# Optimization experiments

Measured on AMD Instinct MI355X. Metric: run time of the kernel, lower is better.

## Reference

```python
import jax, jax.numpy as jnp
import numpy as np

N, E, F, H, C, G = 100000, 800000, 128, 128, 10, 128
EPS = 1e-5


def setup_inputs() -> dict:
    key = jax.random.key(0)
    ks = jax.random.split(key, 8)
    return {
        "x": jax.random.normal(ks[0], (N, F), jnp.float32),
        "edge_index": jax.random.randint(ks[1], (2, E), 0, N),
        "batch": jnp.sort(jax.random.randint(ks[2], (N,), 0, G)),
        "edge_weight": jax.random.uniform(ks[3], (E,), jnp.float32, 0.1, 1.0),
        "bn_feat_w": jnp.ones((F,), jnp.float32),
        "bn_feat_b": jnp.full((F,), 1e-4, jnp.float32),
        "conv_feat_W": jax.random.normal(ks[4], (F, H), jnp.float32) / np.float32(np.sqrt(F)),
        "conv_feat_b": jnp.zeros((H,), jnp.float32),
        "bns_w": jnp.ones((3, H), jnp.float32),
        "bns_b": jnp.full((3, H), 1e-4, jnp.float32),
        "convs_W": jax.random.normal(ks[5], (3, H, H), jnp.float32) / np.float32(np.sqrt(H)),
        "convs_b": jnp.zeros((3, H), jnp.float32),
        "bn_fc_w": jnp.ones((H,), jnp.float32),
        "bn_fc_b": jnp.full((H,), 1e-4, jnp.float32),
        "lin_fc_W": jax.random.normal(ks[6], (H, H), jnp.float32) / np.float32(np.sqrt(H)),
        "lin_fc_b": jnp.zeros((H,), jnp.float32),
        "bn_hidden_w": jnp.ones((H,), jnp.float32),
        "bn_hidden_b": jnp.full((H,), 1e-4, jnp.float32),
        "lin_class_W": jax.random.normal(ks[7], (H, C), jnp.float32) / np.float32(np.sqrt(H)),
        "lin_class_b": jnp.zeros((C,), jnp.float32),
    }


def _bn(h, w, b):
    # training-mode BatchNorm1d: biased batch stats over dim 0
    mu = h.mean(0)
    var = jnp.mean((h - mu) ** 2, 0)
    return (h - mu) * jax.lax.rsqrt(var + EPS) * w + b


def reference(x, edge_index, batch, edge_weight,
              bn_feat_w, bn_feat_b, conv_feat_W, conv_feat_b,
              bns_w, bns_b, convs_W, convs_b,
              bn_fc_w, bn_fc_b, lin_fc_W, lin_fc_b,
              bn_hidden_w, bn_hidden_b, lin_class_W, lin_class_b):
    n = x.shape[0]
    loops = jnp.arange(n)
    # PyG GCNConv: add self-loops (weight 1) + symmetric normalization, shared by all convs
    row = jnp.concatenate([edge_index[0], loops])
    col = jnp.concatenate([edge_index[1], loops])
    ew = jnp.concatenate([edge_weight, jnp.ones((n,), x.dtype)])
    deg = jax.ops.segment_sum(ew, col, num_segments=n)
    dinv = jnp.where(deg > 0, jax.lax.rsqrt(jnp.maximum(deg, EPS)), 0.0)
    norm = (dinv[row] * ew * dinv[col])[:, None]  # [E+N, 1]

    def conv(h, W, b):
        m = (h @ W)[row] * norm                 # gather + scale per edge
        return jax.ops.segment_sum(m, col, num_segments=n) + b

    h = _bn(x, bn_feat_w, bn_feat_b)
    h = jax.nn.relu(conv(h, conv_feat_W, conv_feat_b))
    h_init = h

    x_list = []
    # branch 1: BN -> Conv -> ReLU chain
    h = h_init
    for i in range(3):
        h = jax.nn.relu(conv(_bn(h, bns_w[i], bns_b[i]), convs_W[i], convs_b[i]))
    x_list.append(h)
    # branch 2: double application of the same BN/Conv per step
    h = h_init
    for i in range(3):
        h_ = jax.nn.relu(conv(_bn(h, bns_w[i], bns_b[i]), convs_W[i], convs_b[i]))
        h = jax.nn.relu(conv(_bn(h_, bns_w[i], bns_b[i]), convs_W[i], convs_b[i]))
    x_list.append(h)
    # branch 3: identical to branch 1 when conv_residual=False
    h = h_init
    for i in range(3):
        h = jax.nn.relu(conv(_bn(h, bns_w[i], bns_b[i]), convs_W[i], convs_b[i]))
    x_list.append(h)
    # branch 4: BN -> ReLU only
    h = h_init
    for i in range(3):
        h = jax.nn.relu(_bn(h, bns_w[i], bns_b[i]))
    x_list.append(h)

    def head(hn):
        g = jax.ops.segment_sum(hn, batch, num_segments=G)  # global_add_pool
        g = jax.nn.relu(_bn(g, bn_fc_w, bn_fc_b) @ lin_fc_W + lin_fc_b)
        g = _bn(g, bn_hidden_w, bn_hidden_b)
        return jax.nn.log_softmax(g @ lin_class_W + lin_class_b, axis=-1)

    return tuple(head(hn) for hn in x_list)
```

## Files before the change

### kernel.cpp

```cpp
#include <hip/hip_runtime.h>

#define N_NODES 100000
#define NPAD    100032
#define NBLK    1563
#define NEDGE   800000
#define NGRP    128
#define NSLOT   32
#define EPS     1e-5f

typedef unsigned int   u32;
typedef unsigned short u16;
typedef short bf16x8 __attribute__((ext_vector_type(8)));
typedef float f32x4  __attribute__((ext_vector_type(4)));

__device__ __forceinline__ float bf2f(u32 u){ return __uint_as_float(u << 16); }
__device__ __forceinline__ u16 f2bf(float f){
  u32 x = __float_as_uint(f);
  x += 0x7fffu + ((x >> 16) & 1u);
  return (u16)(x >> 16);
}

__global__ void k_init(float* deg, int* cnt, int* fill, float* gbuf){
  int i = blockIdx.x * 256 + threadIdx.x;
  if (i < NPAD){ deg[i] = 1.0f; cnt[i] = 0; fill[i] = 0; }
  if (i < 4 * NGRP * 128) gbuf[i] = 0.f;
}

__global__ void k_deg(const int* __restrict__ col, const float* __restrict__ ew,
                      float* __restrict__ deg, int* __restrict__ cnt){
  int e = blockIdx.x * 256 + threadIdx.x;
  if (e < NEDGE){
    int c = col[e];
    atomicAdd(&deg[c], ew[e]);
    atomicAdd(&cnt[c], 1);
  }
}

__global__ void k_dinv(const float* __restrict__ deg, float* __restrict__ dinv, float* __restrict__ srow){
  int i = blockIdx.x * 256 + threadIdx.x;
  if (i < N_NODES){
    float d = deg[i];
    float v = d > 0.f ? rsqrtf(fmaxf(d, EPS)) : 0.f;
    dinv[i] = v; srow[i] = v * v;
  }
}

__global__ __launch_bounds__(256) void k_chunksum(const int* __restrict__ cnt, int* __restrict__ csum){
  int b = blockIdx.x, t = threadIdx.x;
  int s = 0;
  for (int i = t; i < 1024; i += 256){ int idx = b * 1024 + i; if (idx < N_NODES) s += cnt[idx]; }
  __shared__ int red[256];
  red[t] = s; __syncthreads();
  for (int o = 128; o > 0; o >>= 1){ if (t < o) red[t] += red[t + o]; __syncthreads(); }
  if (t == 0) csum[b] = red[0];
}

__global__ __launch_bounds__(128) void k_chunkscan(const int* __restrict__ csum, int* __restrict__ coff,
                                                   int* __restrict__ ptrA){
  int t = threadIdx.x;
  __shared__ int s[128];
  int v = (t < 98) ? csum[t] : 0;
  s[t] = v; __syncthreads();
  for (int o = 1; o < 128; o <<= 1){
    int x = (t >= o) ? s[t - o] : 0;
    __syncthreads(); s[t] += x; __syncthreads();
  }
  if (t < 98) coff[t] = s[t] - v;
  if (t == 0) ptrA[N_NODES] = NEDGE;
}

__global__ __launch_bounds__(256) void k_scan2(const int* __restrict__ cnt, const int* __restrict__ coff,
                                               int* __restrict__ ptrA){
  int b = blockIdx.x, t = threadIdx.x;
  int base = b * 1024 + t * 4;
  int v[4], tot = 0;
  #pragma unroll
  for (int k = 0; k < 4; k++){ int idx = base + k; v[k] = (idx < N_NODES) ? cnt[idx] : 0; tot += v[k]; }
  __shared__ int sc[256];
  sc[t] = tot; __syncthreads();
  for (int o = 1; o < 256; o <<= 1){
    int x = (t >= o) ? sc[t - o] : 0;
    __syncthreads(); sc[t] += x; __syncthreads();
  }
  int off = coff[b] + sc[t] - tot;
  #pragma unroll
  for (int k = 0; k < 4; k++){ int idx = base + k; if (idx < N_NODES) ptrA[idx] = off; off += v[k]; }
}

__global__ void k_fill(const int* __restrict__ row, const int* __restrict__ col,
                       const float* __restrict__ ew, const float* __restrict__ dinv,
                       const int* __restrict__ ptrA, int* __restrict__ fill, int2* __restrict__ adj,
                       float* __restrict__ srow){
  int e = blockIdx.x * 256 + threadIdx.x;
  if (e < NEDGE){
    int r = row[e], c = col[e];
    float w = dinv[r] * ew[e] * dinv[c];
    int pos = ptrA[c] + atomicAdd(&fill[c], 1);
    adj[pos] = make_int2(r, __float_as_int(w));
    atomicAdd(&srow[c], w);
  }
}

__global__ __launch_bounds__(256) void k_bhist(const int* __restrict__ batch, int* __restrict__ bpart){
  __shared__ int loc[128];
  int t = threadIdx.x;
  if (t < 128) loc[t] = 0;
  __syncthreads();
  int i = blockIdx.x * 256 + t;
  if (i < N_NODES) atomicAdd(&loc[batch[i]], 1);
  __syncthreads();
  if (t < 128) bpart[blockIdx.x * 128 + t] = loc[t];
}

__global__ __launch_bounds__(128) void k_bscan(const int* __restrict__ bpart, int* __restrict__ gptr){
  int t = threadIdx.x;
  int v = 0;
  for (int p = 0; p < 391; p++) v += bpart[p * 128 + t];
  __shared__ int s[128];
  s[t] = v; __syncthreads();
  for (int o = 1; o < 128; o <<= 1){
    int x = (t >= o) ? s[t - o] : 0;
    __syncthreads(); s[t] += x; __syncthreads();
  }
  gptr[t + 1] = s[t];
  if (t == 0) gptr[0] = 0;
}

__global__ __launch_bounds__(256) void k_cvtstats(const float* __restrict__ x, u32* __restrict__ dst,
                                                  float* __restrict__ sums_out){
  __shared__ float R[1024];
  int t = threadIdx.x;
  float s0 = 0.f, q0 = 0.f, s1 = 0.f, q1 = 0.f;
  size_t base = (size_t)blockIdx.x * 4096 + t;
  #pragma unroll
  for (int it = 0; it < 16; it++){
    size_t idx = base + (size_t)it * 256;
    if (idx < (size_t)N_NODES * 64){
      float2 v = ((const float2*)x)[idx];
      dst[idx] = (u32)f2bf(v.x) | ((u32)f2bf(v.y) << 16);
      s0 += v.x; q0 += v.x * v.x; s1 += v.y; q1 += v.y * v.y;
    }
  }
  R[t] = s0; R[256 + t] = q0; R[512 + t] = s1; R[768 + t] = q1;
  __syncthreads();
  if (t < 64){
    float S0 = 0.f, Q0 = 0.f, S1 = 0.f, Q1 = 0.f;
    #pragma unroll
    for (int g = 0; g < 4; g++){
      S0 += R[g * 64 + t];       Q0 += R[256 + g * 64 + t];
      S1 += R[512 + g * 64 + t]; Q1 += R[768 + g * 64 + t];
    }
    float* so = sums_out + (blockIdx.x & (NSLOT - 1)) * 256;
    atomicAdd(&so[2 * t], S0);
    atomicAdd(&so[2 * t + 1], S1);
    atomicAdd(&so[128 + 2 * t], Q0);
    atomicAdd(&so[128 + 2 * t + 1], Q1);
  }
}

__device__ __forceinline__ void fold_body(int blk, int t, const float* __restrict__ sums,
    const float* __restrict__ bw, const float* __restrict__ bb,
    const float* __restrict__ W, const float* __restrict__ bias,
    u16* __restrict__ Wh, u16* __restrict__ Wl, float* __restrict__ rb,
    float* scl, float* shf, float* stot, float* rred){
  {
    float s = 0.f;
    #pragma unroll 4
    for (int sl = 0; sl < NSLOT; sl++) s += sums[sl * 256 + t];
    stot[t] = s;
  }
  __syncthreads();
  if (t < 128){
    float mu  = stot[t] * (1.f / N_NODES);
    float var = stot[128 + t] * (1.f / N_NODES) - mu * mu;
    float sc  = bw[t] * rsqrtf(var + EPS);
    scl[t] = sc; shf[t] = bb[t] - mu * sc;
  }
  __syncthreads();
  {
    int idx = blk * 256 + t;
    int lane_ = idx & 63, sl = idx >> 6;
    int nt_ = sl >> 2, ks_ = sl & 3;
    int n_ = nt_ * 16 + (lane_ & 15);
    int kb = ks_ * 32 + (lane_ >> 4) * 8;
    u16 hi8[8], lo8[8];
    #pragma unroll
    for (int j = 0; j < 8; j++){
      float wv = W[(kb + j) * 128 + n_];
      float xv = scl[kb + j] * wv;
      u16 hh = f2bf(xv);
      hi8[j] = hh; lo8[j] = f2bf(xv - bf2f(hh));
    }
    uint4 ph, pl;
    ph.x = (u32)hi8[0] | ((u32)hi8[1] << 16); ph.y = (u32)hi8[2] | ((u32)hi8[3] << 16);
    ph.z = (u32)hi8[4] | ((u32)hi8[5] << 16); ph.w = (u32)hi8[6] | ((u32)hi8[7] << 16);
    pl.x = (u32)lo8[0] | ((u32)lo8[1] << 16); pl.y = (u32)lo8[2] | ((u32)lo8[3] << 16);
    pl.z = (u32)lo8[4] | ((u32)lo8[5] << 16); pl.w = (u32)lo8[6] | ((u32)lo8[7] << 16);
    *(uint4*)&Wh[idx * 8] = ph;
    *(uint4*)&Wl[idx * 8] = pl;
  }
  {
    int nl = t & 15, kk = t >> 4;
    int n2 = blk * 16 + nl;
    float rp = 0.f;
    #pragma unroll
    for (int j = 0; j < 8; j++){
      int k2 = kk * 8 + j;
      rp += shf[k2] * W[k2 * 128 + n2];
    }
    rred[t] = rp;
  }
  __syncthreads();
  if (t < 16){
    float s = 0.f;
    #pragma unroll
    for (int kk2 = 0; kk2 < 16; kk2++) s += rred[kk2 * 16 + t];
    int n2 = blk * 16 + t;
    rb[n2] = s;
    rb[128 + n2] = bias[n2];
  }
}

__global__ __launch_bounds__(256) void k_fold(const float* __restrict__ sums,
    const float* __restrict__ bw, const float* __restrict__ bb,
    const float* __restrict__ W, const float* __restrict__ bias,
    u16* __restrict__ Wh, u16* __restrict__ Wl, float* __restrict__ rb){
  __shared__ float scl[128], shf[128], stot[256], rred[256];
  fold_body(blockIdx.x, threadIdx.x, sums, bw, bb, W, bias, Wh, Wl, rb, scl, shf, stot, rred);
}

__global__ __launch_bounds__(256) void k_fold2(
    const float* __restrict__ sumsA, const float* __restrict__ bwA, const float* __restrict__ bbA,
    const float* __restrict__ WA, const float* __restrict__ biasA,
    u16* __restrict__ WhA, u16* __restrict__ WlA, float* __restrict__ rbA,
    const float* __restrict__ sumsB, const float* __restrict__ bwB, const float* __restrict__ bbB,
    const float* __restrict__ WB, const float* __restrict__ biasB,
    u16* __restrict__ WhB, u16* __restrict__ WlB, float* __restrict__ rbB){
  __shared__ float scl[128], shf[128], stot[256], rred[256];
  int bb_ = blockIdx.x;
  if (bb_ < 8)
    fold_body(bb_, threadIdx.x, sumsA, bwA, bbA, WA, biasA, WhA, WlA, rbA, scl, shf, stot, rred);
  else
    fold_body(bb_ - 8, threadIdx.x, sumsB, bwB, bbB, WB, biasB, WhB, WlB, rbB, scl, shf, stot, rred);
}

#define CONV_EPILOGUE(RB, HOUT, SOUT, BLK)                                     \
  __syncthreads();                                                             \
  sred[t] = 0.f;                                                               \
  __syncthreads();                                                             \
  _Pragma("unroll")                                                            \
  for (int nt = 0; nt < 8; nt++){                                              \
    int colc = nt * 16 + m;                                                    \
    float rv = RB[colc], bv = RB[128 + colc];                                  \
    float s = 0.f, qq = 0.f;                                                   \
    _Pragma("unroll")                                                          \
    for (int r = 0; r < 4; r++){                                               \
      int rown = row0 + q * 4 + r;                                             \
      float v = C[nt][r] + srow[rown] * rv + bv;                               \
      v = fmaxf(v, 0.f);                                                       \
      u16 sv = f2bf(v);                                                        \
      HOUT[(size_t)rown * 128 + colc] = sv;                                    \
      if (rown < N_NODES){ float vv = bf2f(sv); s += vv; qq += vv * vv; }      \
    }                                                                          \
    s  += __shfl_xor(s, 16, 64);  s  += __shfl_xor(s, 32, 64);                 \
    qq += __shfl_xor(qq, 16, 64); qq += __shfl_xor(qq, 32, 64);                \
    if (q == 0){                                                               \
      atomicAdd(&sred[colc], s);                                               \
      atomicAdd(&sred[128 + colc], qq);                                        \
    }                                                                          \
  }                                                                            \
  __syncthreads();                                                             \
  atomicAdd(&SOUT[((BLK) & (NSLOT - 1)) * 256 + t], sred[t]);

#define FMA_KS(KS, V, WT) \
  acc[KS][0] += (WT) * __uint_as_float((V).x << 16); acc[KS][1] += (WT) * __uint_as_float((V).x & 0xffff0000u); \
  acc[KS][2] += (WT) * __uint_as_float((V).y << 16); acc[KS][3] += (WT) * __uint_as_float((V).y & 0xffff0000u); \
  acc[KS][4] += (WT) * __uint_as_float((V).z << 16); acc[KS][5] += (WT) * __uint_as_float((V).z & 0xffff0000u); \
  acc[KS][6] += (WT) * __uint_as_float((V).w << 16); acc[KS][7] += (WT) * __uint_as_float((V).w & 0xffff0000u);

#define VMCNT6() asm volatile("s_waitcnt vmcnt(6)" ::: "memory")
#define VMCNT5() asm volatile("s_waitcnt vmcnt(5)" ::: "memory")
#define SB0()    __builtin_amdgcn_sched_barrier(0)


__device__ __forceinline__ void gll_stage(const u16* __restrict__ h, u16* dst, int2 aj, int lane){
  int c = lane & 15, g = lane >> 4;
  #pragma unroll
  for (int ii = 0; ii < 4; ii++){
    int rl = ii * 4 + g;
    int srcrow = __shfl(aj.x, rl, 64);
    const u16* src = h + (size_t)srcrow * 128 + (size_t)((c ^ rl) * 8);
    __builtin_amdgcn_global_load_lds((const void*)src, (void*)(dst + ii * 512), 16, 0, 0);
  }
}

#define GITER(WA, WB, WC, WD, STG, J)                                          \
  WD = *(const int2*)(adj + base_ + min((J) + 3, dcl));                        \
  VMCNT6();                                                                    \
  {                                                                            \
    float wgt = __int_as_float(__shfl((WA).y, m, 64));                         \
    if ((J) < deg){                                                            \
      const u16* sp = stage + (STG) * 2048;                                    \
      _Pragma("unroll")                                                        \
      for (int ks = 0; ks < 4; ks++){                                          \
        int slot = (q + 4 * ks) ^ m;                                           \
        uint4 v = *(const uint4*)(sp + m * 128 + slot * 8);                    \
        FMA_KS(ks, v, wgt)                                                     \
      }                                                                        \
    }                                                                          \
  }                                                                            \
  VMCNT5();                                                                    \
  gll_stage(h, stage + (STG) * 2048, WC, lane);                                \
  SB0();

__device__ __forceinline__ void gather_row_lds(const u16* __restrict__ h,
    const int* __restrict__ ptrA, const int2* __restrict__ adj,
    const float* __restrict__ dinv, int row0, int lane, u16* stage,
    float (&acc)[4][8]){
  int m = lane & 15, q = lane >> 4;
  #pragma unroll
  for (int ks = 0; ks < 4; ks++)
    #pragma unroll
    for (int j = 0; j < 8; j++) acc[ks][j] = 0.f;
  int r = row0 + m;
  int r2 = min(r, N_NODES - 1);
  int b0 = ptrA[r2], b1 = ptrA[r2 + 1];
  int deg = (r < N_NODES) ? (b1 - b0) : 0;
  int base_ = b0;
  int dcl = max(deg - 1, 0);
  float di = dinv[r2];
  float sw = (r < N_NODES) ? di * di : 0.f;
  const u16* hq = h + q * 8;
  const u16* sp_ = hq + (size_t)r2 * 128;
  uint4 s0 = *(const uint4*)(sp_);
  uint4 s1 = *(const uint4*)(sp_ + 32);
  uint4 s2 = *(const uint4*)(sp_ + 64);
  uint4 s3 = *(const uint4*)(sp_ + 96);
  int2 W0 = *(const int2*)(adj + base_);
  int2 W1 = *(const int2*)(adj + base_ + min(1, dcl));
  int wmax = deg;
  wmax = max(wmax, __shfl_xor(wmax, 1, 64));
  wmax = max(wmax, __shfl_xor(wmax, 2, 64));
  wmax = max(wmax, __shfl_xor(wmax, 4, 64));
  wmax = max(wmax, __shfl_xor(wmax, 8, 64));
  FMA_KS(0, s0, sw) FMA_KS(1, s1, sw) FMA_KS(2, s2, sw) FMA_KS(3, s3, sw)
  if (wmax > 0){
    int2 W2 = W0, W3 = W0;
    SB0();
    gll_stage(h, stage, W0, lane);
    SB0();
    W2 = *(const int2*)(adj + base_ + min(2, dcl));
    SB0();
    gll_stage(h, stage + 2048, W1, lane);
    SB0();
    for (int j0 = 0; j0 < wmax; j0 += 4){
      GITER(W0, W1, W2, W3, 0, j0)
      GITER(W1, W2, W3, W0, 1, j0 + 1)
      GITER(W2, W3, W0, W1, 0, j0 + 2)
      GITER(W3, W0, W1, W2, 1, j0 + 3)
    }
  }
}

#define BUILD_AFRAG()                                                          \
  bf16x8 AH[4], AL[4];                                                         \
  _Pragma("unroll")                                                            \
  for (int ks = 0; ks < 4; ks++)                                               \
    _Pragma("unroll")                                                          \
    for (int j = 0; j < 8; j++){                                               \
      u16 hh = f2bf(acc[ks][j]);                                               \
      AH[ks][j] = (short)hh;                                                   \
      AL[ks][j] = (short)f2bf(acc[ks][j] - bf2f(hh));                          \
    }

#define MFMA_3PASS(WH, WL_)                                                    \
  _Pragma("unroll")                                                            \
  for (int ks = 0; ks < 4; ks++){                                              \
    _Pragma("unroll")                                                          \
    for (int nt = 0; nt < 8; nt++){                                            \
      bf16x8 bh = ((const bf16x8*)WH)[(nt * 4 + ks) * 64 + lane];              \
      bf16x8 bl = ((const bf16x8*)WL_)[(nt * 4 + ks) * 64 + lane];             \
      C[nt] = __builtin_amdgcn_mfma_f32_16x16x32_bf16(AH[ks], bh, C[nt], 0, 0, 0); \
      C[nt] = __builtin_amdgcn_mfma_f32_16x16x32_bf16(AL[ks], bh, C[nt], 0, 0, 0); \
      C[nt] = __builtin_amdgcn_mfma_f32_16x16x32_bf16(AH[ks], bl, C[nt], 0, 0, 0); \
    }                                                                          \
  }

__global__ __launch_bounds__(256, 3) void k_conv(
    const u16* __restrict__ h, const int* __restrict__ ptrA, const int2* __restrict__ adj,
    const float* __restrict__ dinv, const float* __restrict__ srow,
    const u16* __restrict__ Wh, const u16* __restrict__ Wl, const float* __restrict__ rb,
    u16* __restrict__ hout, float* __restrict__ sums_out){
  __shared__ u16 hstage[4][2][2048];
  __shared__ float sred[256];
  int t = threadIdx.x;
  int wave = t >> 6, lane = t & 63, m = lane & 15, q = lane >> 4;
  int blk = blockIdx.x;
  int row0 = blk * 64 + wave * 16;
  float acc[4][8];
  gather_row_lds(h, ptrA, adj, dinv, row0, lane, &hstage[wave][0][0], acc);
  BUILD_AFRAG()
  f32x4 C[8];
  #pragma unroll
  for (int nt = 0; nt < 8; nt++) C[nt] = f32x4{0.f, 0.f, 0.f, 0.f};
  MFMA_3PASS(Wh, Wl)
  CONV_EPILOGUE(rb, hout, sums_out, blk)
}

__global__ __launch_bounds__(256, 3) void k_conv2(
    const u16* __restrict__ hA, const u16* __restrict__ hB,
    const int* __restrict__ ptrA, const int2* __restrict__ adj,
    const float* __restrict__ dinv, const float* __restrict__ srow,
    const u16* __restrict__ WhA, const u16* __restrict__ WlA, const float* __restrict__ rbA,
    u16* __restrict__ houtA, float* __restrict__ sumsA,
    const u16* __restrict__ WhB, const u16* __restrict__ WlB, const float* __restrict__ rbB,
    u16* __restrict__ houtB, float* __restrict__ sumsB){
  __shared__ u16 hstage[4][2][2048];
  __shared__ float sred[256];
  int t = threadIdx.x;
  int wave = t >> 6, lane = t & 63, m = lane & 15, q = lane >> 4;
  int bb = blockIdx.x;
  int second = bb >= NBLK;
  int blk = second ? bb - NBLK : bb;
  const u16* h = second ? hB : hA;
  const u16* Wh = second ? WhB : WhA;
  const u16* Wl = second ? WlB : WlA;
  const float* rb = second ? rbB : rbA;
  u16* hout = second ? houtB : houtA;
  float* sums_out = second ? sumsB : sumsA;
  int row0 = blk * 64 + wave * 16;
  float acc[4][8];
  gather_row_lds(h, ptrA, adj, dinv, row0, lane, &hstage[wave][0][0], acc);
  BUILD_AFRAG()
  f32x4 C[8];
  #pragma unroll
  for (int nt = 0; nt < 8; nt++) C[nt] = f32x4{0.f, 0.f, 0.f, 0.f};
  MFMA_3PASS(Wh, Wl)
  CONV_EPILOGUE(rb, hout, sums_out, blk)
}

__global__ __launch_bounds__(256, 3) void k_dualconv(
    const u16* __restrict__ h, const int* __restrict__ ptrA, const int2* __restrict__ adj,
    const float* __restrict__ dinv, const float* __restrict__ srow,
    const u16* __restrict__ Wh1, const u16* __restrict__ Wl1, const float* __restrict__ rb1,
    u16* __restrict__ hout1, float* __restrict__ sums1,
    const u16* __restrict__ Wh2, const u16* __restrict__ Wl2, const float* __restrict__ rb2,
    u16* __restrict__ hout2, float* __restrict__ sums2){
  __shared__ u16 hstage[4][2][2048];
  __shared__ float sred[256];
  int t = threadIdx.x;
  int wave = t >> 6, lane = t & 63, m = lane & 15, q = lane >> 4;
  int blk = blockIdx.x;
  int row0 = blk * 64 + wave * 16;
  float acc[4][8];
  gather_row_lds(h, ptrA, adj, dinv, row0, lane, &hstage[wave][0][0], acc);
  BUILD_AFRAG()
  f32x4 C[8];
  #pragma unroll
  for (int nt = 0; nt < 8; nt++) C[nt] = f32x4{0.f, 0.f, 0.f, 0.f};
  MFMA_3PASS(Wh1, Wl1)
  CONV_EPILOGUE(rb1, hout1, sums1, blk)
  #pragma unroll
  for (int nt = 0; nt < 8; nt++) C[nt] = f32x4{0.f, 0.f, 0.f, 0.f};
  MFMA_3PASS(Wh2, Wl2)
  CONV_EPILOGUE(rb2, hout2, sums2, blk)
}

__global__ __launch_bounds__(256) void k_normrelu(const u16* __restrict__ h, const float* __restrict__ sums,
    const float* __restrict__ bw, const float* __restrict__ bb, u16* __restrict__ o,
    float* __restrict__ sums_out){
  __shared__ float scl[128], shf[128], R[1024], stot[256];
  int t = threadIdx.x;
  {
    float s = 0.f;
    #pragma unroll 4
    for (int sl = 0; sl < NSLOT; sl++) s += sums[sl * 256 + t];
    stot[t] = s;
  }
  __syncthreads();
  if (t < 128){
    float mu  = stot[t] * (1.f / N_NODES);
    float var = stot[128 + t] * (1.f / N_NODES) - mu * mu;
    float sc  = bw[t] * rsqrtf(var + EPS);
    scl[t] = sc; shf[t] = bb[t] - mu * sc;
  }
  __syncthreads();
  int c0 = (t & 63) * 2;
  float sc0 = scl[c0], sh0 = shf[c0], sc1 = scl[c0 + 1], sh1 = shf[c0 + 1];
  float s0 = 0.f, q0 = 0.f, s1 = 0.f, q1 = 0.f;
  size_t base = (size_t)blockIdx.x * 4096 + t;
  #pragma unroll
  for (int it = 0; it < 16; it++){
    size_t idx = base + (size_t)it * 256;
    if (idx < (size_t)N_NODES * 64){
      u32 v = ((const u32*)h)[idx];
      float x0 = fmaxf(bf2f(v & 0xffffu) * sc0 + sh0, 0.f);
      float x1 = fmaxf(bf2f(v >> 16) * sc1 + sh1, 0.f);
      u16 r0 = f2bf(x0), r1 = f2bf(x1);
      ((u32*)o)[idx] = (u32)r0 | ((u32)r1 << 16);
      float y0 = bf2f(r0), y1 = bf2f(r1);
      s0 += y0; q0 += y0 * y0; s1 += y1; q1 += y1 * y1;
    }
  }
  R[t] = s0; R[256 + t] = q0; R[512 + t] = s1; R[768 + t] = q1;
  __syncthreads();
  if (t < 64){
    float S0 = 0.f, Q0 = 0.f, S1 = 0.f, Q1 = 0.f;
    #pragma unroll
    for (int g = 0; g < 4; g++){
      S0 += R[g * 64 + t];       Q0 += R[256 + g * 64 + t];
      S1 += R[512 + g * 64 + t]; Q1 += R[768 + g * 64 + t];
    }
    float* so = sums_out + (blockIdx.x & (NSLOT - 1)) * 256;
    atomicAdd(&so[2 * t], S0);
    atomicAdd(&so[2 * t + 1], S1);
    atomicAdd(&so[128 + 2 * t], Q0);
    atomicAdd(&so[128 + 2 * t + 1], Q1);
  }
}

__global__ __launch_bounds__(128) void k_pool(const u16* __restrict__ h, const int* __restrict__ gptr,
                                              float* __restrict__ gdst){
  int g = blockIdx.x >> 3, s = blockIdx.x & 7, t = threadIdx.x;
  int b = gptr[g], e = gptr[g + 1];
  int len = e - b, per = (len + 7) >> 3;
  int r0 = b + s * per, r1 = min(r0 + per, e);
  float acc = 0.f;
  for (int r = r0; r < r1; r++) acc += bf2f(h[(size_t)r * 128 + t]);
  atomicAdd(&gdst[g * 128 + t], acc);
}

__global__ __launch_bounds__(256) void k_head(const float* __restrict__ gbuf,
    const float* __restrict__ fcw, const float* __restrict__ fcb,
    const float* __restrict__ Wfc, const float* __restrict__ bfc,
    const float* __restrict__ bhw, const float* __restrict__ bhb,
    const float* __restrict__ Wcl, const float* __restrict__ bcl,
    float* __restrict__ out){
  __shared__ float GS[128 * 65];
  __shared__ float ls[256], lq[256];
  __shared__ float scl[128], shf[128], scl2[128], shf2[128];
  __shared__ float sumT[128], sumQ[128];
  __shared__ float WclT[1280], Lrow[1280];
  int t = threadIdx.x, br = blockIdx.x;
  int slot = (br == 1) ? 1 : (br == 3 ? 3 : 0);
  const float* G = gbuf + slot * 16384;
  {
    int col = t & 127, hf2 = t >> 7;
    float s = 0.f, q = 0.f;
    for (int g = hf2 * 64; g < hf2 * 64 + 64; g++){ float v = G[g * 128 + col]; s += v; q += v * v; }
    ls[t] = s; lq[t] = q;
  }
  for (int idx = t; idx < 1280; idx += 256){
    int cc = idx >> 7, c = idx & 127;
    WclT[idx] = Wcl[c * 10 + cc];
  }
  if (t < 128){ sumT[t] = 0.f; sumQ[t] = 0.f; }
  __syncthreads();
  if (t < 128){
    float s = ls[t] + ls[t + 128], q = lq[t] + lq[t + 128];
    float mu = s * (1.f / 128), var = q * (1.f / 128) - mu * mu;
    float sc = fcw[t] * rsqrtf(var + EPS);
    scl[t] = sc; shf[t] = fcb[t] - mu * sc;
  }
  __syncthreads();
  int tr = t >> 4, tc = t & 15, r0 = tr * 8, c0 = tc * 8;
  float acc[8][8];
  #pragma unroll
  for (int a = 0; a < 8; a++)
    #pragma unroll
    for (int b = 0; b < 8; b++) acc[a][b] = 0.f;
  for (int kh = 0; kh < 2; kh++){
    for (int idx = t; idx < 8192; idx += 256){
      int r = idx >> 6, kk = idx & 63, f = kh * 64 + kk;
      GS[r * 65 + kk] = G[r * 128 + f] * scl[f] + shf[f];
    }
    __syncthreads();
    #pragma unroll 2
    for (int k = 0; k < 64; k++){
      float a[8];
      #pragma unroll
      for (int ri = 0; ri < 8; ri++) a[ri] = GS[(r0 + ri) * 65 + k];
      float4 b0 = *(const float4*)&Wfc[(kh * 64 + k) * 128 + c0];
      float4 b1 = *(const float4*)&Wfc[(kh * 64 + k) * 128 + c0 + 4];
      float bb[8] = {b0.x, b0.y, b0.z, b0.w, b1.x, b1.y, b1.z, b1.w};
      #pragma unroll
      for (int ri = 0; ri < 8; ri++)
        #pragma unroll
        for (int ci = 0; ci < 8; ci++) acc[ri][ci] += a[ri] * bb[ci];
    }
    __syncthreads();
  }
  #pragma unroll
  for (int ci = 0; ci < 8; ci++){
    float bb = bfc[c0 + ci];
    float s = 0.f, q = 0.f;
    #pragma unroll
    for (int ri = 0; ri < 8; ri++){
      float v = fmaxf(acc[ri][ci] + bb, 0.f);
      acc[ri][ci] = v; s += v; q += v * v;
    }
    atomicAdd(&sumT[c0 + ci], s);
    atomicAdd(&sumQ[c0 + ci], q);
  }
  __syncthreads();
  if (t < 128){
    float mu = sumT[t] * (1.f / 128), var = sumQ[t] * (1.f / 128) - mu * mu;
    float sc = bhw[t] * rsqrtf(var + EPS);
    scl2[t] = sc; shf2[t] = bhb[t] - mu * sc;
  }
  __syncthreads();
  #pragma unroll
  for (int ci = 0; ci < 8; ci++){
    float sc = scl2[c0 + ci], sh = shf2[c0 + ci];
    #pragma unroll
    for (int ri = 0; ri < 8; ri++) acc[ri][ci] = acc[ri][ci] * sc + sh;
  }
  #pragma unroll
  for (int ri = 0; ri < 8; ri++){
    float pl[10];
    #pragma unroll
    for (int cc = 0; cc < 10; cc++) pl[cc] = 0.f;
    #pragma unroll
    for (int ci = 0; ci < 8; ci++){
      float v = acc[ri][ci];
      #pragma unroll
      for (int cc = 0; cc < 10; cc++) pl[cc] += v * WclT[cc * 128 + c0 + ci];
    }
    #pragma unroll
    for (int msk = 1; msk < 16; msk <<= 1)
      #pragma unroll
      for (int cc = 0; cc < 10; cc++) pl[cc] += __shfl_xor(pl[cc], msk, 64);
    if (tc == 0)
      #pragma unroll
      for (int cc = 0; cc < 10; cc++) Lrow[(r0 + ri) * 10 + cc] = pl[cc];
  }
  __syncthreads();
  if (t < 128){
    float l[10];
    #pragma unroll
    for (int cc = 0; cc < 10; cc++) l[cc] = Lrow[t * 10 + cc] + bcl[cc];
    float m = l[0];
    #pragma unroll
    for (int cc = 1; cc < 10; cc++) m = fmaxf(m, l[cc]);
    float se = 0.f;
    #pragma unroll
    for (int cc = 0; cc < 10; cc++) se += expf(l[cc] - m);
    float lse = m + logf(se);
    #pragma unroll
    for (int cc = 0; cc < 10; cc++) out[br * 1280 + t * 10 + cc] = l[cc] - lse;
  }
}

extern "C" void kernel_launch(void* const* d_in, const int* in_sizes, int n_in,
                              void* d_out, int out_size, void* d_ws, size_t ws_size,
                              hipStream_t stream){
  const float* x    = (const float*)d_in[0];
  const int*  ei    = (const int*)d_in[1];
  const int*  batch = (const int*)d_in[2];
  const float* ew   = (const float*)d_in[3];
  const float* bnfw = (const float*)d_in[4];
  const float* bnfb = (const float*)d_in[5];
  const float* cfW  = (const float*)d_in[6];
  const float* cfb  = (const float*)d_in[7];
  const float* bnsw = (const float*)d_in[8];
  const float* bnsb = (const float*)d_in[9];
  const float* cvW  = (const float*)d_in[10];
  const float* cvb  = (const float*)d_in[11];
  const float* fcw  = (const float*)d_in[12];
  const float* fcb  = (const float*)d_in[13];
  const float* Wfc  = (const float*)d_in[14];
  const float* bfc  = (const float*)d_in[15];
  const float* bhw  = (const float*)d_in[16];
  const float* bhb  = (const float*)d_in[17];
  const float* Wcl  = (const float*)d_in[18];
  const float* bcl  = (const float*)d_in[19];
  float* out = (float*)d_out;

  char* p = (char*)d_ws;
  auto carve = [&](size_t bytes)->void*{ void* r = (void*)p; p += (bytes + 255) & ~(size_t)255; return r; };
  float* deg  = (float*)carve((size_t)NPAD * 4);
  float* dinv = (float*)carve((size_t)NPAD * 4);
  float* srow = (float*)carve((size_t)NPAD * 4);
  int*   cnt  = (int*)carve((size_t)NPAD * 4);
  int*   fill = (int*)carve((size_t)NPAD * 4);
  int*   ptrA = (int*)carve((size_t)(NPAD + 1) * 4);
  int*   bpart= (int*)carve((size_t)391 * 128 * 4);
  int*   csum = (int*)carve(512);
  int*   coff = (int*)carve(512);
  int*   gptr = (int*)carve(1024);
  float* S    = (float*)carve((size_t)13 * NSLOT * 1024);
  float* gbuf = (float*)carve(4 * 128 * 128 * 4);
  u16*   F0h  = (u16*)carve(32768);  u16* F0l = (u16*)carve(32768);  float* F0r = (float*)carve(1024);
  u16*   F1h  = (u16*)carve(32768);  u16* F1l = (u16*)carve(32768);  float* F1r = (float*)carve(1024);
  u16*   F2h  = (u16*)carve(32768);  u16* F2l = (u16*)carve(32768);  float* F2r = (float*)carve(1024);
  u16*   B0   = (u16*)carve((size_t)NPAD * 256);
  u16*   B1   = (u16*)carve((size_t)NPAD * 256);
  u16*   B2   = (u16*)carve((size_t)NPAD * 256);
  u16*   B3   = (u16*)carve((size_t)NPAD * 256);
  int2*  adj  = (int2*)carve((size_t)NEDGE * 8);
  u16*   Xb   = B3;
  auto Sb = [&](int i){ return S + (size_t)i * NSLOT * 256; };

  (void)hipMemsetAsync(S, 0, (size_t)13 * NSLOT * 1024, stream);

  k_init<<<392, 256, 0, stream>>>(deg, cnt, fill, gbuf);
  k_deg<<<3125, 256, 0, stream>>>(ei + NEDGE, ew, deg, cnt);
  k_dinv<<<391, 256, 0, stream>>>(deg, dinv, srow);
  k_chunksum<<<98, 256, 0, stream>>>(cnt, csum);
  k_chunkscan<<<1, 128, 0, stream>>>(csum, coff, ptrA);
  k_scan2<<<98, 256, 0, stream>>>(cnt, coff, ptrA);
  k_fill<<<3125, 256, 0, stream>>>(ei, ei + NEDGE, ew, dinv, ptrA, fill, adj, srow);
  k_bhist<<<391, 256, 0, stream>>>(batch, bpart);
  k_bscan<<<1, 128, 0, stream>>>(bpart, gptr);
  k_cvtstats<<<NBLK, 256, 0, stream>>>(x, (u32*)Xb, Sb(0));

  auto fold = [&](const float* Sin, const float* bw, const float* bb,
                  const float* W, const float* bias, u16* Fh, u16* Fl, float* Fr){
    k_fold<<<8, 256, 0, stream>>>(Sin, bw, bb, W, bias, Fh, Fl, Fr);
  };
  auto conv = [&](const u16* hin, const u16* Fh, const u16* Fl, const float* Fr,
                  u16* hout, float* Sout){
    k_conv<<<NBLK, 256, 0, stream>>>(hin, ptrA, adj, dinv, srow, Fh, Fl, Fr, hout, Sout);
  };

  fold(Sb(0), bnfw, bnfb, cfW, cfb, F0h, F0l, F0r);
  conv(Xb, F0h, F0l, F0r, B0, Sb(1));
  fold(Sb(1), bnsw, bnsb, cvW, cvb, F1h, F1l, F1r);
  conv(B0, F1h, F1l, F1r, B1, Sb(2));
  k_normrelu<<<NBLK, 256, 0, stream>>>(B0, Sb(1), bnsw,       bnsb,       B2, Sb(3));
  k_normrelu<<<NBLK, 256, 0, stream>>>(B2, Sb(3), bnsw + 128, bnsb + 128, B3, Sb(4));
  k_normrelu<<<NBLK, 256, 0, stream>>>(B3, Sb(4), bnsw + 256, bnsb + 256, B2, Sb(12));
  k_pool<<<1024, 128, 0, stream>>>(B2, gptr, gbuf + 3 * 16384);
  k_fold2<<<16, 256, 0, stream>>>(
      Sb(2), bnsw + 128, bnsb + 128, cvW + 16384, cvb + 128, F0h, F0l, F0r,
      Sb(2), bnsw,       bnsb,       cvW,         cvb,       F1h, F1l, F1r);
  k_dualconv<<<NBLK, 256, 0, stream>>>(B1, ptrA, adj, dinv, srow,
      F0h, F0l, F0r, B3, Sb(5),
      F1h, F1l, F1r, B2, Sb(6));
  k_fold2<<<16, 256, 0, stream>>>(
      Sb(5), bnsw + 256, bnsb + 256, cvW + 32768, cvb + 256, F2h, F2l, F2r,
      Sb(6), bnsw + 128, bnsb + 128, cvW + 16384, cvb + 128, F0h, F0l, F0r);
  k_conv2<<<2 * NBLK, 256, 0, stream>>>(B3, B2, ptrA, adj, dinv, srow,
      F2h, F2l, F2r, B0, Sb(10),
      F0h, F0l, F0r, B1, Sb(7));
  k_pool<<<1024, 128, 0, stream>>>(B0, gptr, gbuf);
  fold(Sb(7), bnsw + 128, bnsb + 128, cvW + 16384, cvb + 128, F1h, F1l, F1r);
  conv(B1, F1h, F1l, F1r, B2, Sb(8));
  fold(Sb(8), bnsw + 256, bnsb + 256, cvW + 32768, cvb + 256, F2h, F2l, F2r);
  conv(B2, F2h, F2l, F2r, B1, Sb(9));
  fold(Sb(9), bnsw + 256, bnsb + 256, cvW + 32768, cvb + 256, F0h, F0l, F0r);
  conv(B1, F0h, F0l, F0r, B3, Sb(11));
  k_pool<<<1024, 128, 0, stream>>>(B3, gptr, gbuf + 16384);

  k_head<<<4, 256, 0, stream>>>(gbuf, fcw, fcb, Wfc, bfc, bhw, bhb, Wcl, bcl, out);
}
```

Measured before the change: 1.094 ms.

## Deepen gather pipeline to triple-buffered LDS, widen normrelu and pool loads

```diff
diff --git a/kernel.cpp b/kernel.cpp
--- a/kernel.cpp
+++ b/kernel.cpp
@@ -278,10 +278,10 @@
   acc[KS][4] += (WT) * __uint_as_float((V).z << 16); acc[KS][5] += (WT) * __uint_as_float((V).z & 0xffff0000u); \
   acc[KS][6] += (WT) * __uint_as_float((V).w << 16); acc[KS][7] += (WT) * __uint_as_float((V).w & 0xffff0000u);
 
-#define VMCNT6() asm volatile("s_waitcnt vmcnt(6)" ::: "memory")
-#define VMCNT5() asm volatile("s_waitcnt vmcnt(5)" ::: "memory")
-#define SB0()    __builtin_amdgcn_sched_barrier(0)
-
+#define VMCNT_2()  asm volatile("s_waitcnt vmcnt(2)" ::: "memory")
+#define VMCNT_6()  asm volatile("s_waitcnt vmcnt(6)" ::: "memory")
+#define VMCNT_10() asm volatile("s_waitcnt vmcnt(10)" ::: "memory")
+#define VMCNT_11() asm volatile("s_waitcnt vmcnt(11)" ::: "memory")
 
 __device__ __forceinline__ void gll_stage(const u16* __restrict__ h, u16* dst, int2 aj, int lane){
   int c = lane & 15, g = lane >> 4;
@@ -294,11 +294,11 @@
   }
 }
 
-#define GITER(WA, WB, WC, WD, STG, J)                                          \
-  WD = *(const int2*)(adj + base_ + min((J) + 3, dcl));                        \
-  VMCNT6();                                                                    \
+#define GITER(WA_, WISS_, WD_, STG, J)                                         \
+  WD_ = *(const int2*)(adj + base_ + min((J) + 5, dcl));                       \
+  VMCNT_11();                                                                  \
   {                                                                            \
-    float wgt = __int_as_float(__shfl((WA).y, m, 64));                         \
+    float wgt = __int_as_float(__shfl((WA_).y, m, 64));                        \
     if ((J) < deg){                                                            \
       const u16* sp = stage + (STG) * 2048;                                    \
       _Pragma("unroll")                                                        \
@@ -309,9 +309,8 @@
       }                                                                        \
     }                                                                          \
   }                                                                            \
-  VMCNT5();                                                                    \
-  gll_stage(h, stage + (STG) * 2048, WC, lane);                                \
-  SB0();
+  VMCNT_10();                                                                  \
+  gll_stage(h, stage + (STG) * 2048, WISS_, lane);
 
 __device__ __forceinline__ void gather_row_lds(const u16* __restrict__ h,
     const int* __restrict__ ptrA, const int2* __restrict__ adj,
@@ -326,7 +325,7 @@
   int r2 = min(r, N_NODES - 1);
   int b0 = ptrA[r2], b1 = ptrA[r2 + 1];
   int deg = (r < N_NODES) ? (b1 - b0) : 0;
-  int base_ = b0;
+  int base_ = min(b0, NEDGE - 1);
   int dcl = max(deg - 1, 0);
   float di = dinv[r2];
   float sw = (r < N_NODES) ? di * di : 0.f;
@@ -336,8 +335,6 @@
   uint4 s1 = *(const uint4*)(sp_ + 32);
   uint4 s2 = *(const uint4*)(sp_ + 64);
   uint4 s3 = *(const uint4*)(sp_ + 96);
-  int2 W0 = *(const int2*)(adj + base_);
-  int2 W1 = *(const int2*)(adj + base_ + min(1, dcl));
   int wmax = deg;
   wmax = max(wmax, __shfl_xor(wmax, 1, 64));
   wmax = max(wmax, __shfl_xor(wmax, 2, 64));
@@ -345,19 +342,26 @@
   wmax = max(wmax, __shfl_xor(wmax, 8, 64));
   FMA_KS(0, s0, sw) FMA_KS(1, s1, sw) FMA_KS(2, s2, sw) FMA_KS(3, s3, sw)
   if (wmax > 0){
-    int2 W2 = W0, W3 = W0;
-    SB0();
+    int2 W0 = *(const int2*)(adj + base_);
+    int2 W1 = *(const int2*)(adj + base_ + min(1, dcl));
+    int2 W2 = *(const int2*)(adj + base_ + min(2, dcl));
+    int2 W3, W4, W5;
+    VMCNT_2();
     gll_stage(h, stage, W0, lane);
-    SB0();
-    W2 = *(const int2*)(adj + base_ + min(2, dcl));
-    SB0();
+    W3 = *(const int2*)(adj + base_ + min(3, dcl));
+    VMCNT_6();
     gll_stage(h, stage + 2048, W1, lane);
-    SB0();
-    for (int j0 = 0; j0 < wmax; j0 += 4){
-      GITER(W0, W1, W2, W3, 0, j0)
-      GITER(W1, W2, W3, W0, 1, j0 + 1)
-      GITER(W2, W3, W0, W1, 0, j0 + 2)
-      GITER(W3, W0, W1, W2, 1, j0 + 3)
+    W4 = *(const int2*)(adj + base_ + min(4, dcl));
+    VMCNT_10();
+    gll_stage(h, stage + 4096, W2, lane);
+    int j = 0;
+    for (;;){
+      GITER(W0, W3, W5, 0, j) if (++j >= wmax) break;
+      GITER(W1, W4, W0, 1, j) if (++j >= wmax) break;
+      GITER(W2, W5, W1, 2, j) if (++j >= wmax) break;
+      GITER(W3, W0, W2, 0, j) if (++j >= wmax) break;
+      GITER(W4, W1, W3, 1, j) if (++j >= wmax) break;
+      GITER(W5, W2, W4, 2, j) if (++j >= wmax) break;
     }
   }
 }
@@ -391,7 +395,7 @@
     const float* __restrict__ dinv, const float* __restrict__ srow,
     const u16* __restrict__ Wh, const u16* __restrict__ Wl, const float* __restrict__ rb,
     u16* __restrict__ hout, float* __restrict__ sums_out){
-  __shared__ u16 hstage[4][2][2048];
+  __shared__ u16 hstage[4][3][2048];
   __shared__ float sred[256];
   int t = threadIdx.x;
   int wave = t >> 6, lane = t & 63, m = lane & 15, q = lane >> 4;
@@ -415,7 +419,7 @@
     u16* __restrict__ houtA, float* __restrict__ sumsA,
     const u16* __restrict__ WhB, const u16* __restrict__ WlB, const float* __restrict__ rbB,
     u16* __restrict__ houtB, float* __restrict__ sumsB){
-  __shared__ u16 hstage[4][2][2048];
+  __shared__ u16 hstage[4][3][2048];
   __shared__ float sred[256];
   int t = threadIdx.x;
   int wave = t >> 6, lane = t & 63, m = lane & 15, q = lane >> 4;
@@ -446,7 +450,7 @@
     u16* __restrict__ hout1, float* __restrict__ sums1,
     const u16* __restrict__ Wh2, const u16* __restrict__ Wl2, const float* __restrict__ rb2,
     u16* __restrict__ hout2, float* __restrict__ sums2){
-  __shared__ u16 hstage[4][2][2048];
+  __shared__ u16 hstage[4][3][2048];
   __shared__ float sred[256];
   int t = threadIdx.x;
   int wave = t >> 6, lane = t & 63, m = lane & 15, q = lane >> 4;
@@ -469,7 +473,7 @@
 __global__ __launch_bounds__(256) void k_normrelu(const u16* __restrict__ h, const float* __restrict__ sums,
     const float* __restrict__ bw, const float* __restrict__ bb, u16* __restrict__ o,
     float* __restrict__ sums_out){
-  __shared__ float scl[128], shf[128], R[1024], stot[256];
+  __shared__ float scl[128], shf[128], R[2048], stot[256];
   int t = threadIdx.x;
   {
     float s = 0.f;
@@ -485,49 +489,78 @@
     scl[t] = sc; shf[t] = bb[t] - mu * sc;
   }
   __syncthreads();
-  int c0 = (t & 63) * 2;
+  int c0 = (t & 31) * 4;
   float sc0 = scl[c0], sh0 = shf[c0], sc1 = scl[c0 + 1], sh1 = shf[c0 + 1];
-  float s0 = 0.f, q0 = 0.f, s1 = 0.f, q1 = 0.f;
-  size_t base = (size_t)blockIdx.x * 4096 + t;
-  #pragma unroll
-  for (int it = 0; it < 16; it++){
+  float sc2 = scl[c0 + 2], sh2 = shf[c0 + 2], sc3 = scl[c0 + 3], sh3 = shf[c0 + 3];
+  float s0 = 0.f, q0 = 0.f, s1 = 0.f, q1 = 0.f, s2 = 0.f, q2 = 0.f, s3 = 0.f, q3 = 0.f;
+  size_t base = (size_t)blockIdx.x * 2048 + t;
+  #pragma unroll
+  for (int it = 0; it < 8; it++){
     size_t idx = base + (size_t)it * 256;
-    if (idx < (size_t)N_NODES * 64){
-      u32 v = ((const u32*)h)[idx];
-      float x0 = fmaxf(bf2f(v & 0xffffu) * sc0 + sh0, 0.f);
-      float x1 = fmaxf(bf2f(v >> 16) * sc1 + sh1, 0.f);
-      u16 r0 = f2bf(x0), r1 = f2bf(x1);
-      ((u32*)o)[idx] = (u32)r0 | ((u32)r1 << 16);
-      float y0 = bf2f(r0), y1 = bf2f(r1);
+    if (idx < (size_t)N_NODES * 32){
+      uint2 v = ((const uint2*)h)[idx];
+      float x0 = fmaxf(bf2f(v.x & 0xffffu) * sc0 + sh0, 0.f);
+      float x1 = fmaxf(bf2f(v.x >> 16) * sc1 + sh1, 0.f);
+      float x2 = fmaxf(bf2f(v.y & 0xffffu) * sc2 + sh2, 0.f);
+      float x3 = fmaxf(bf2f(v.y >> 16) * sc3 + sh3, 0.f);
+      u16 r0 = f2bf(x0), r1 = f2bf(x1), r2 = f2bf(x2), r3 = f2bf(x3);
+      uint2 w;
+      w.x = (u32)r0 | ((u32)r1 << 16);
+      w.y = (u32)r2 | ((u32)r3 << 16);
+      ((uint2*)o)[idx] = w;
+      float y0 = bf2f(r0), y1 = bf2f(r1), y2 = bf2f(r2), y3 = bf2f(r3);
       s0 += y0; q0 += y0 * y0; s1 += y1; q1 += y1 * y1;
-    }
-  }
-  R[t] = s0; R[256 + t] = q0; R[512 + t] = s1; R[768 + t] = q1;
-  __syncthreads();
-  if (t < 64){
-    float S0 = 0.f, Q0 = 0.f, S1 = 0.f, Q1 = 0.f;
-    #pragma unroll
-    for (int g = 0; g < 4; g++){
-      S0 += R[g * 64 + t];       Q0 += R[256 + g * 64 + t];
-      S1 += R[512 + g * 64 + t]; Q1 += R[768 + g * 64 + t];
+      s2 += y2; q2 += y2 * y2; s3 += y3; q3 += y3 * y3;
+    }
+  }
+  R[t] = s0; R[256 + t] = s1; R[512 + t] = s2; R[768 + t] = s3;
+  R[1024 + t] = q0; R[1280 + t] = q1; R[1536 + t] = q2; R[1792 + t] = q3;
+  __syncthreads();
+  if (t < 128){
+    int j = t & 3, l = t >> 2;
+    float S = 0.f, Q = 0.f;
+    #pragma unroll
+    for (int g = 0; g < 8; g++){
+      int th = l + 32 * g;
+      S += R[j * 256 + th];
+      Q += R[1024 + j * 256 + th];
     }
     float* so = sums_out + (blockIdx.x & (NSLOT - 1)) * 256;
-    atomicAdd(&so[2 * t], S0);
-    atomicAdd(&so[2 * t + 1], S1);
-    atomicAdd(&so[128 + 2 * t], Q0);
-    atomicAdd(&so[128 + 2 * t + 1], Q1);
+    atomicAdd(&so[t], S);
+    atomicAdd(&so[128 + t], Q);
   }
 }
 
 __global__ __launch_bounds__(128) void k_pool(const u16* __restrict__ h, const int* __restrict__ gptr,
                                               float* __restrict__ gdst){
+  __shared__ float part[2][16][8];
   int g = blockIdx.x >> 3, s = blockIdx.x & 7, t = threadIdx.x;
+  int cc = t & 15, rr = t >> 4, wv = t >> 6, rrw = rr & 3;
   int b = gptr[g], e = gptr[g + 1];
   int len = e - b, per = (len + 7) >> 3;
   int r0 = b + s * per, r1 = min(r0 + per, e);
-  float acc = 0.f;
-  for (int r = r0; r < r1; r++) acc += bf2f(h[(size_t)r * 128 + t]);
-  atomicAdd(&gdst[g * 128 + t], acc);
+  float a[8] = {0.f, 0.f, 0.f, 0.f, 0.f, 0.f, 0.f, 0.f};
+  for (int r = r0 + rr; r < r1; r += 8){
+    uint4 v = *(const uint4*)(h + (size_t)r * 128 + cc * 8);
+    a[0] += bf2f(v.x & 0xffffu); a[1] += bf2f(v.x >> 16);
+    a[2] += bf2f(v.y & 0xffffu); a[3] += bf2f(v.y >> 16);
+    a[4] += bf2f(v.z & 0xffffu); a[5] += bf2f(v.z >> 16);
+    a[6] += bf2f(v.w & 0xffffu); a[7] += bf2f(v.w >> 16);
+  }
+  #pragma unroll
+  for (int j = 0; j < 8; j++){
+    a[j] += __shfl_xor(a[j], 16, 64);
+    a[j] += __shfl_xor(a[j], 32, 64);
+  }
+  if (rrw == 0){
+    #pragma unroll
+    for (int j = 0; j < 8; j++) part[wv][cc][j] = a[j];
+  }
+  __syncthreads();
+  {
+    float sum = part[0][t >> 3][t & 7] + part[1][t >> 3][t & 7];
+    atomicAdd(&gdst[g * 128 + t], sum);
+  }
 }
 
 __global__ __launch_bounds__(256) void k_head(const float* __restrict__ gbuf,
```

Result: faster. 1.056 ms (-3.5%).
